# Kernel tuning notes

Hardware: AMD Instinct MI355X
Metric: run time of the kernel (lower is better)

The kernel has to match this reference:

```python
import jax, jax.numpy as jnp
import numpy as np

B = 16384
D = 64            # bottom_mlp_layers[-1] = embedding_dim
DENSE = 512
HIST = 50         # history length per row
C_CAMP = 1000     # num_collisions for campaign table (sqrt(1e6))
C_FEAT = 316      # num_collisions for 1e5-vocab tables
NQ_CAMP = 1000    # ceil(1e6/1000)
NQ_FEAT = 317     # ceil(1e5/316)
NFEAT = 7
N = NFEAT + 1 + 1 # sparse features + dense row
PROJ = 128


def setup_inputs() -> dict:
    key = jax.random.key(0)
    ks = jax.random.split(key, 20)
    inp = {
        'x': jax.random.normal(ks[0], (B, DENSE), jnp.float32),
        'hist_idx': jax.random.randint(ks[1], (B * HIST,), 0, 1000000),
        'hist_offsets': jnp.arange(B, dtype=jnp.int64) * HIST,
        'feat_idx': jax.random.randint(ks[2], (B, NFEAT), 0, 100000),
        # QR embedding tables (quotient, remainder)
        'Wq_c': jax.random.normal(ks[3], (NQ_CAMP, D), jnp.float32) * 0.05,
        'Wr_c': jax.random.normal(ks[4], (C_CAMP, D), jnp.float32) * 0.05,
        'Wq_f': jax.random.normal(ks[5], (NFEAT, NQ_FEAT, D), jnp.float32) * 0.05,
        'Wr_f': jax.random.normal(ks[6], (NFEAT, C_FEAT, D), jnp.float32) * 0.05,
        # bottom MLP: 512->512 relu 512->256 relu 256->64
        'W0': jax.random.normal(ks[7], (512, DENSE), jnp.float32) * 0.03,
        'b0': jnp.zeros((512,), jnp.float32),
        'W1': jax.random.normal(ks[8], (256, 512), jnp.float32) * 0.04,
        'b1': jnp.zeros((256,), jnp.float32),
        'W2': jax.random.normal(ks[9], (64, 256), jnp.float32) * 0.06,
        'b2': jnp.zeros((64,), jnp.float32),
        # projection: (D + (N^2-N)/2) -> PROJ ; 64 + 36 = 100
        'Wp': jax.random.normal(ks[10], (PROJ, D + (N * N - N) // 2), jnp.float32) * 0.1,
        'bp': jnp.zeros((PROJ,), jnp.float32),
    }
    return inp


def _forward(x, hist_idx, hist_offsets, feat_idx, Wq_c, Wr_c, Wq_f, Wr_f,
             W0, b0, W1, b1, W2, b2, Wp, bp):
    # bottom MLP
    h = jax.nn.relu(x @ W0.T + b0)
    h = jax.nn.relu(h @ W1.T + b1)
    dense = h @ W2.T + b2                                   # [B, D]

    # QR embedding bag (mode='mean', operation='mult') for history feature
    e = Wq_c[hist_idx // C_CAMP] * Wr_c[hist_idx % C_CAMP]  # [M, D]
    M = hist_idx.shape[0]
    seg = jnp.cumsum(jnp.zeros((M,), jnp.int32).at[hist_offsets].add(1)) - 1
    sums = jax.ops.segment_sum(e, seg, num_segments=B)      # [B, D]
    counts = jnp.diff(jnp.concatenate([hist_offsets, jnp.array([M], hist_offsets.dtype)]))
    hist_emb = sums / counts[:, None].astype(sums.dtype)

    # single-valued QR lookups (bag size 1 -> mean == lookup)
    t = jnp.arange(NFEAT)[None, :]
    fe = Wq_f[t, feat_idx // C_FEAT] * Wr_f[t, feat_idx % C_FEAT]  # [B, NFEAT, D]

    # pairwise dot interaction: upper triangle (offset=1) of T @ T^T
    T = jnp.concatenate([dense[:, None, :], hist_emb[:, None, :], fe], axis=1)  # [B, N, D]
    Z = jnp.einsum('bnd,bmd->bnm', T, T)
    row, col = np.triu_indices(N, k=1)
    Z_flat = Z[:, row, col]                                  # [B, (N^2-N)/2]

    combined = jnp.concatenate([dense, Z_flat], axis=1)
    return combined @ Wp.T + bp                              # [B, PROJ]


def reference(x, hist_idx, hist_offsets, feat_idx, Wq_c, Wr_c, Wq_f, Wr_f,
              W0, b0, W1, b1, W2, b2, Wp, bp):
    return _forward(x, hist_idx, hist_offsets, feat_idx, Wq_c, Wr_c, Wq_f, Wr_f,
                    W0, b0, W1, b1, W2, b2, Wp, bp)
```

## Files before the change

kernel.cpp:

```cpp
#include <hip/hip_runtime.h>
#include <hip/hip_bf16.h>
#include <stdint.h>

#define DENSE_D 512
#define HIDDEN1 512
#define HIDDEN2 256
#define EMB_D   64
#define NFEAT   7
#define NROWS   9
#define NPAIRS  36
#define COMB    100
#define KPROJ   128
#define PROJ    128
#define C_CAMP  1000
#define C_FEAT  316
#define NQ_FEAT 317

typedef __attribute__((ext_vector_type(8))) __bf16 bf16x8;
typedef __attribute__((ext_vector_type(8))) unsigned short ushort8;
typedef __attribute__((ext_vector_type(4))) float  facc4;

#define GLD_LDS16(gp, lp) __builtin_amdgcn_global_load_lds( \
    (__attribute__((address_space(1))) void*)(gp), \
    (__attribute__((address_space(3))) void*)(lp), 16, 0, 0)

__device__ inline unsigned short f2bf(float f) {
    __hip_bfloat16 h = __float2bfloat16(f);
    return *reinterpret_cast<unsigned short*>(&h);
}
__device__ inline float blo(unsigned int u) { return __uint_as_float(u << 16); }
__device__ inline float bhi(unsigned int u) { return __uint_as_float(u & 0xffff0000u); }

template<int BM, int BN, int WM, int WN, bool RELU, bool OUT_BF16, bool A_F32>
__global__ __launch_bounds__(WM * WN * 64)
void gemm_bf16(const void* __restrict__ Avoid,
               const __hip_bfloat16* __restrict__ W,
               const float* __restrict__ bias,
               void* __restrict__ Cout,
               int M, int N, int K)
{
    constexpr int BK      = 32;
    constexpr int THREADS = WM * WN * 64;
    constexpr int MREP    = BM / (WM * 16);
    constexpr int NREP    = BN / (WN * 16);
    constexpr int ACH     = BM * BK / 8;
    constexpr int BCH     = BN * BK / 8;

    __shared__ __align__(16) __hip_bfloat16 Asm[BK / 8][BM][8];
    __shared__ __align__(16) __hip_bfloat16 Bsm[BK / 8][BN][8];

    const int tid  = threadIdx.x;
    const int lane = tid & 63;
    const int wave = tid >> 6;
    const int wm   = wave / WN;
    const int wn   = wave % WN;
    const int row0 = blockIdx.x * BM;
    const int col0 = blockIdx.y * BN;
    const int fr   = lane & 15;
    const int fk   = lane >> 4;

    facc4 acc[MREP][NREP] = {};

    for (int k0 = 0; k0 < K; k0 += BK) {
        if (A_F32) {
            const float* Af = (const float*)Avoid;
            for (int p = tid; p < ACH; p += THREADS) {
                const int r  = p & (BM - 1);
                const int kc = p / BM;
                const float* src = Af + (size_t)(row0 + r) * K + k0 + kc * 8;
                const float4 v0 = *reinterpret_cast<const float4*>(src);
                const float4 v1 = *reinterpret_cast<const float4*>(src + 4);
                ushort8 cv;
                cv[0] = f2bf(v0.x); cv[1] = f2bf(v0.y);
                cv[2] = f2bf(v0.z); cv[3] = f2bf(v0.w);
                cv[4] = f2bf(v1.x); cv[5] = f2bf(v1.y);
                cv[6] = f2bf(v1.z); cv[7] = f2bf(v1.w);
                *reinterpret_cast<ushort8*>(
                    (unsigned short*)(&Asm[0][0][0]) + (size_t)p * 8) = cv;
            }
        } else {
            const __hip_bfloat16* Ab = (const __hip_bfloat16*)Avoid;
            for (int p = tid; p < ACH; p += THREADS) {
                const int r  = p & (BM - 1);
                const int kc = p / BM;
                GLD_LDS16(Ab + (size_t)(row0 + r) * K + k0 + kc * 8,
                          (&Asm[0][0][0]) + (size_t)p * 8);
            }
        }
        for (int p = tid; p < BCH; p += THREADS) {
            const int r  = p & (BN - 1);
            const int kc = p / BN;
            GLD_LDS16(W + (size_t)(col0 + r) * K + k0 + kc * 8,
                      (&Bsm[0][0][0]) + (size_t)p * 8);
        }
        __syncthreads();

        bf16x8 af[MREP], bw[NREP];
        #pragma unroll
        for (int m = 0; m < MREP; ++m)
            af[m] = *reinterpret_cast<const bf16x8*>(
                &Asm[fk][wm * (MREP * 16) + m * 16 + fr][0]);
        #pragma unroll
        for (int n = 0; n < NREP; ++n)
            bw[n] = *reinterpret_cast<const bf16x8*>(
                &Bsm[fk][wn * (NREP * 16) + n * 16 + fr][0]);
        #pragma unroll
        for (int m = 0; m < MREP; ++m)
            #pragma unroll
            for (int n = 0; n < NREP; ++n)
                acc[m][n] = __builtin_amdgcn_mfma_f32_16x16x32_bf16(
                    af[m], bw[n], acc[m][n], 0, 0, 0);
        __syncthreads();
    }

    #pragma unroll
    for (int n = 0; n < NREP; ++n) {
        const int col = col0 + wn * (NREP * 16) + n * 16 + fr;
        const float bv = bias[col];
        #pragma unroll
        for (int m = 0; m < MREP; ++m) {
            #pragma unroll
            for (int j = 0; j < 4; ++j) {
                const int row = row0 + wm * (MREP * 16) + m * 16 + fk * 4 + j;
                float v = acc[m][n][j] + bv;
                if (RELU) v = fmaxf(v, 0.f);
                if (OUT_BF16)
                    ((__hip_bfloat16*)Cout)[(size_t)row * N + col] = __float2bfloat16(v);
                else
                    ((float*)Cout)[(size_t)row * N + col] = v;
            }
        }
    }
}

__device__ inline void cast_seg(const float* __restrict__ src,
                                unsigned short* __restrict__ dst,
                                int n4, int id, int stride)
{
    for (int i = id; i < n4; i += stride) {
        const float4 v = reinterpret_cast<const float4*>(src)[i];
        ushort4 o;
        o.x = f2bf(v.x); o.y = f2bf(v.y); o.z = f2bf(v.z); o.w = f2bf(v.w);
        reinterpret_cast<ushort4*>(dst)[i] = o;
    }
}

__global__ __launch_bounds__(256)
void prep_all(const float* __restrict__ W0, const float* __restrict__ W1,
              const float* __restrict__ W2, const float* __restrict__ Wp,
              const float* __restrict__ Wq_c, const float* __restrict__ Wr_c,
              const float* __restrict__ Wq_f, const float* __restrict__ Wr_f,
              unsigned short* w0b, unsigned short* w1b, unsigned short* w2b,
              unsigned short* wpb, unsigned short* qcb, unsigned short* rcb,
              unsigned short* qfb, unsigned short* rfb)
{
    const int id = blockIdx.x * blockDim.x + threadIdx.x;
    const int stride = gridDim.x * blockDim.x;
    cast_seg(W0,   w0b, HIDDEN1 * DENSE_D / 4, id, stride);
    cast_seg(W1,   w1b, HIDDEN2 * HIDDEN1 / 4, id, stride);
    cast_seg(W2,   w2b, EMB_D * HIDDEN2 / 4,   id, stride);
    cast_seg(Wq_c, qcb, C_CAMP * EMB_D / 4,    id, stride);
    cast_seg(Wr_c, rcb, C_CAMP * EMB_D / 4,    id, stride);
    cast_seg(Wq_f, qfb, NFEAT * NQ_FEAT * EMB_D / 4, id, stride);
    cast_seg(Wr_f, rfb, NFEAT * C_FEAT * EMB_D / 4,  id, stride);
    for (int i = id; i < PROJ * KPROJ; i += stride) {
        const int r = i >> 7, c = i & 127;
        wpb[i] = (c < COMB) ? f2bf(Wp[r * COMB + c]) : (unsigned short)0;
    }
}

__global__ __launch_bounds__(256)
void tail_fused(const unsigned short* __restrict__ h1b,
                const unsigned short* __restrict__ w2b,
                const float* __restrict__ b2,
                const int* __restrict__ hist_idx,
                const int* __restrict__ hist_off,
                const int* __restrict__ feat_idx,
                const unsigned short* __restrict__ qcb,
                const unsigned short* __restrict__ rcb,
                const unsigned short* __restrict__ qfb,
                const unsigned short* __restrict__ rfb,
                const unsigned short* __restrict__ wpb,
                const float* __restrict__ bp,
                float* __restrict__ out,
                int B, int Mtot)
{
    const int r0   = blockIdx.x * 32;
    const int t    = threadIdx.x;
    const int lane = t & 63;
    const int wave = t >> 6;
    const int wm   = wave >> 1;
    const int wn   = wave & 1;
    const int fr   = lane & 15;
    const int fk   = lane >> 4;

    __shared__ unsigned short T[32][NROWS][68];
    __shared__ unsigned short combs[32][136];

    {
        facc4 acc[2] = {};
        const unsigned short* arow = h1b + (size_t)(r0 + wm * 16 + fr) * HIDDEN2;
        #pragma unroll
        for (int kw = 0; kw < 8; ++kw) {
            const bf16x8 af = *reinterpret_cast<const bf16x8*>(arow + kw * 32 + fk * 8);
            #pragma unroll
            for (int n = 0; n < 2; ++n) {
                const bf16x8 bw = *reinterpret_cast<const bf16x8*>(
                    w2b + (size_t)(wn * 32 + n * 16 + fr) * HIDDEN2 + kw * 32 + fk * 8);
                acc[n] = __builtin_amdgcn_mfma_f32_16x16x32_bf16(af, bw, acc[n], 0, 0, 0);
            }
        }
        #pragma unroll
        for (int n = 0; n < 2; ++n) {
            const int col = wn * 32 + n * 16 + fr;
            const float bv = b2[col];
            #pragma unroll
            for (int j = 0; j < 4; ++j) {
                const int row = wm * 16 + fk * 4 + j;
                const unsigned short hv = f2bf(acc[n][j] + bv);
                T[row][0][col]  = hv;
                combs[row][col] = hv;
            }
        }
    }

    for (int p = t; p < 32 * 18; p += 256) {
        const int row = p / 18, c = p % 18;
        *reinterpret_cast<unsigned int*>(&combs[row][100 + c * 2]) = 0u;
    }

    {
        const int row = t >> 3;
        const int oc  = t & 7;
        const int br  = r0 + row;

        const int fbase = br * NFEAT;
        #pragma unroll
        for (int f = 0; f < NFEAT; ++f) {
            const int fi = feat_idx[fbase + f];
            const int q = fi / C_FEAT, r = fi - q * C_FEAT;
            const unsigned short* qp = qfb + ((size_t)f * NQ_FEAT + q) * EMB_D + oc * 8;
            const unsigned short* rp = rfb + ((size_t)f * C_FEAT  + r) * EMB_D + oc * 8;
            const uint2 qa = *reinterpret_cast<const uint2*>(qp);
            const uint2 qb = *reinterpret_cast<const uint2*>(qp + 4);
            const uint2 ra = *reinterpret_cast<const uint2*>(rp);
            const uint2 rb = *reinterpret_cast<const uint2*>(rp + 4);
            union { ushort8 v; uint2 u[2]; } pk;
            pk.v[0] = f2bf(blo(qa.x) * blo(ra.x));
            pk.v[1] = f2bf(bhi(qa.x) * bhi(ra.x));
            pk.v[2] = f2bf(blo(qa.y) * blo(ra.y));
            pk.v[3] = f2bf(bhi(qa.y) * bhi(ra.y));
            pk.v[4] = f2bf(blo(qb.x) * blo(rb.x));
            pk.v[5] = f2bf(bhi(qb.x) * bhi(rb.x));
            pk.v[6] = f2bf(blo(qb.y) * blo(rb.y));
            pk.v[7] = f2bf(bhi(qb.y) * bhi(rb.y));
            *reinterpret_cast<uint2*>(&T[row][2 + f][oc * 8])     = pk.u[0];
            *reinterpret_cast<uint2*>(&T[row][2 + f][oc * 8 + 4]) = pk.u[1];
        }

        const int start = hist_off[br];
        const int end   = (br + 1 < B) ? hist_off[br + 1] : Mtot;
        const int cnt   = end - start;
        const int* hp = hist_idx + start;
        float a[8] = {};
        #pragma unroll 2
        for (int i = 0; i < cnt; ++i) {
            const int hi = hp[i];
            const int q = hi / C_CAMP, r = hi - q * C_CAMP;
            const unsigned short* qp = qcb + (size_t)q * EMB_D + oc * 8;
            const unsigned short* rp = rcb + (size_t)r * EMB_D + oc * 8;
            const uint2 qa = *reinterpret_cast<const uint2*>(qp);
            const uint2 qb = *reinterpret_cast<const uint2*>(qp + 4);
            const uint2 ra = *reinterpret_cast<const uint2*>(rp);
            const uint2 rb = *reinterpret_cast<const uint2*>(rp + 4);
            a[0] += blo(qa.x) * blo(ra.x); a[1] += bhi(qa.x) * bhi(ra.x);
            a[2] += blo(qa.y) * blo(ra.y); a[3] += bhi(qa.y) * bhi(ra.y);
            a[4] += blo(qb.x) * blo(rb.x); a[5] += bhi(qb.x) * bhi(rb.x);
            a[6] += blo(qb.y) * blo(rb.y); a[7] += bhi(qb.y) * bhi(rb.y);
        }
        const float inv = 1.f / (float)max(cnt, 1);
        union { ushort8 v; uint2 u[2]; } pk;
        #pragma unroll
        for (int k = 0; k < 8; ++k) pk.v[k] = f2bf(a[k] * inv);
        *reinterpret_cast<uint2*>(&T[row][1][oc * 8])     = pk.u[0];
        *reinterpret_cast<uint2*>(&T[row][1][oc * 8 + 4]) = pk.u[1];
    }
    __syncthreads();

    for (int p = t; p < NPAIRS * 32; p += 256) {
        const int row = p & 31;
        const int pr  = p >> 5;
        int i = 0, rem = pr;
        while (rem >= (NROWS - 1) - i) { rem -= (NROWS - 1) - i; ++i; }
        const int j = i + 1 + rem;
        const unsigned short* ti = &T[row][i][0];
        const unsigned short* tj = &T[row][j][0];
        float s = 0.f;
        #pragma unroll
        for (int d = 0; d < EMB_D; d += 4) {
            const uint2 u = *reinterpret_cast<const uint2*>(ti + d);
            const uint2 v = *reinterpret_cast<const uint2*>(tj + d);
            s += blo(u.x) * blo(v.x) + bhi(u.x) * bhi(v.x)
               + blo(u.y) * blo(v.y) + bhi(u.y) * bhi(v.y);
        }
        combs[row][EMB_D + pr] = f2bf(s);
    }
    __syncthreads();

    {
        facc4 acc[4] = {};
        #pragma unroll
        for (int kw = 0; kw < 4; ++kw) {
            const bf16x8 af = *reinterpret_cast<const bf16x8*>(
                &combs[wm * 16 + fr][kw * 32 + fk * 8]);
            #pragma unroll
            for (int n = 0; n < 4; ++n) {
                const bf16x8 bw = *reinterpret_cast<const bf16x8*>(
                    wpb + (size_t)(wn * 64 + n * 16 + fr) * KPROJ + kw * 32 + fk * 8);
                acc[n] = __builtin_amdgcn_mfma_f32_16x16x32_bf16(af, bw, acc[n], 0, 0, 0);
            }
        }
        #pragma unroll
        for (int n = 0; n < 4; ++n) {
            const int col = wn * 64 + n * 16 + fr;
            const float bv = bp[col];
            #pragma unroll
            for (int j = 0; j < 4; ++j) {
                const int row = wm * 16 + fk * 4 + j;
                out[(size_t)(r0 + row) * PROJ + col] = acc[n][j] + bv;
            }
        }
    }
}

extern "C" void kernel_launch(void* const* d_in, const int* in_sizes, int n_in,
                              void* d_out, int out_size, void* d_ws, size_t ws_size,
                              hipStream_t stream)
{
    const float* x        = (const float*)d_in[0];
    const int*   hist_idx = (const int*)  d_in[1];
    const int*   hist_off = (const int*)  d_in[2];
    const int*   feat_idx = (const int*)  d_in[3];
    const float* Wq_c     = (const float*)d_in[4];
    const float* Wr_c     = (const float*)d_in[5];
    const float* Wq_f     = (const float*)d_in[6];
    const float* Wr_f     = (const float*)d_in[7];
    const float* W0       = (const float*)d_in[8];
    const float* b0       = (const float*)d_in[9];
    const float* W1       = (const float*)d_in[10];
    const float* b1       = (const float*)d_in[11];
    const float* W2       = (const float*)d_in[12];
    const float* b2       = (const float*)d_in[13];
    const float* Wp       = (const float*)d_in[14];
    const float* bp       = (const float*)d_in[15];

    const int M    = in_sizes[0] / DENSE_D;
    const int Mtot = in_sizes[1];

    char* w = (char*)d_ws;
    auto take = [&](size_t bytes) { char* p = w; w += (bytes + 255) & ~(size_t)255; return p; };
    unsigned short* w0b = (unsigned short*)take(HIDDEN1 * DENSE_D * 2);
    unsigned short* w1b = (unsigned short*)take(HIDDEN2 * HIDDEN1 * 2);
    unsigned short* w2b = (unsigned short*)take(EMB_D * HIDDEN2 * 2);
    unsigned short* wpb = (unsigned short*)take(PROJ * KPROJ * 2);
    unsigned short* qcb = (unsigned short*)take(C_CAMP * EMB_D * 2);
    unsigned short* rcb = (unsigned short*)take(C_CAMP * EMB_D * 2);
    unsigned short* qfb = (unsigned short*)take(NFEAT * NQ_FEAT * EMB_D * 2);
    unsigned short* rfb = (unsigned short*)take(NFEAT * C_FEAT * EMB_D * 2);
    unsigned short* h0b = (unsigned short*)take((size_t)M * HIDDEN1 * 2);
    unsigned short* h1b = (unsigned short*)take((size_t)M * HIDDEN2 * 2);

    prep_all<<<512, 256, 0, stream>>>(W0, W1, W2, Wp, Wq_c, Wr_c, Wq_f, Wr_f,
                                      w0b, w1b, w2b, wpb, qcb, rcb, qfb, rfb);

    gemm_bf16<128, 256, 2, 4, true, true, true>
        <<<dim3(M / 128, HIDDEN1 / 256), 512, 0, stream>>>(
        x, (const __hip_bfloat16*)w0b, b0, h0b, M, HIDDEN1, DENSE_D);

    gemm_bf16<64, 256, 2, 4, true, true, false>
        <<<dim3(M / 64, HIDDEN2 / 256), 512, 0, stream>>>(
        h0b, (const __hip_bfloat16*)w1b, b1, h1b, M, HIDDEN2, HIDDEN1);

    tail_fused<<<M / 32, 256, 0, stream>>>(
        h1b, w2b, b2, hist_idx, hist_off, feat_idx,
        qcb, rcb, qfb, rfb, wpb, bp, (float*)d_out, M, Mtot);
}
```

Before: 87.67 us.

## Switch MLP GEMMs to 32x32 MFMA full-width tiles and halve tail block rows

The bottom-MLP GEMMs now use 32x32x16 bf16 MFMA. Each block covers the full output width (64 rows by 512 or 256 columns), with the 8 waves split only along N, so the fp32 x tile is loaded and converted once instead of once per column tile. The fused tail kernel now handles 16 rows per block instead of 32, with 16 threads per row for the gathers. This doubles the block count for latency hiding, but each wave does fewer MFMAs per gather. The risk is that larger accumulators (16 floats per fragment, MREP=2 by NREP=2) raise register pressure and may lower occupancy.

```diff
diff --git a/kernel.cpp b/kernel.cpp
--- a/kernel.cpp
+++ b/kernel.cpp
@@ -15,10 +15,12 @@
 #define C_CAMP  1000
 #define C_FEAT  316
 #define NQ_FEAT 317
-
-typedef __attribute__((ext_vector_type(8))) __bf16 bf16x8;
-typedef __attribute__((ext_vector_type(8))) unsigned short ushort8;
-typedef __attribute__((ext_vector_type(4))) float  facc4;
+#define TROWS   16
+
+typedef __attribute__((ext_vector_type(8)))  __bf16 bf16x8;
+typedef __attribute__((ext_vector_type(8)))  unsigned short ushort8;
+typedef __attribute__((ext_vector_type(4)))  float  facc4;
+typedef __attribute__((ext_vector_type(16))) float  facc16;
 
 #define GLD_LDS16(gp, lp) __builtin_amdgcn_global_load_lds( \
     (__attribute__((address_space(1))) void*)(gp), \
@@ -31,18 +33,18 @@
 __device__ inline float blo(unsigned int u) { return __uint_as_float(u << 16); }
 __device__ inline float bhi(unsigned int u) { return __uint_as_float(u & 0xffff0000u); }
 
-template<int BM, int BN, int WM, int WN, bool RELU, bool OUT_BF16, bool A_F32>
-__global__ __launch_bounds__(WM * WN * 64)
-void gemm_bf16(const void* __restrict__ Avoid,
-               const __hip_bfloat16* __restrict__ W,
-               const float* __restrict__ bias,
-               void* __restrict__ Cout,
-               int M, int N, int K)
+template<int BM, int BN, int WN, bool RELU, bool OUT_BF16, bool A_F32>
+__global__ __launch_bounds__(WN * 64)
+void gemm32(const void* __restrict__ Avoid,
+            const __hip_bfloat16* __restrict__ W,
+            const float* __restrict__ bias,
+            void* __restrict__ Cout,
+            int M, int N, int K)
 {
     constexpr int BK      = 32;
-    constexpr int THREADS = WM * WN * 64;
-    constexpr int MREP    = BM / (WM * 16);
-    constexpr int NREP    = BN / (WN * 16);
+    constexpr int THREADS = WN * 64;
+    constexpr int MREP    = BM / 32;
+    constexpr int NREP    = BN / (WN * 32);
     constexpr int ACH     = BM * BK / 8;
     constexpr int BCH     = BN * BK / 8;
 
@@ -52,14 +54,12 @@
     const int tid  = threadIdx.x;
     const int lane = tid & 63;
     const int wave = tid >> 6;
-    const int wm   = wave / WN;
-    const int wn   = wave % WN;
     const int row0 = blockIdx.x * BM;
     const int col0 = blockIdx.y * BN;
-    const int fr   = lane & 15;
-    const int fk   = lane >> 4;
-
-    facc4 acc[MREP][NREP] = {};
+    const int fr   = lane & 31;
+    const int fh   = lane >> 5;
+
+    facc16 acc[MREP][NREP] = {};
 
     for (int k0 = 0; k0 < K; k0 += BK) {
         if (A_F32) {
@@ -95,34 +95,39 @@
         }
         __syncthreads();
 
-        bf16x8 af[MREP], bw[NREP];
-        #pragma unroll
-        for (int m = 0; m < MREP; ++m)
-            af[m] = *reinterpret_cast<const bf16x8*>(
-                &Asm[fk][wm * (MREP * 16) + m * 16 + fr][0]);
-        #pragma unroll
-        for (int n = 0; n < NREP; ++n)
-            bw[n] = *reinterpret_cast<const bf16x8*>(
-                &Bsm[fk][wn * (NREP * 16) + n * 16 + fr][0]);
-        #pragma unroll
-        for (int m = 0; m < MREP; ++m)
+        bf16x8 af[2][MREP], bw[2][NREP];
+        #pragma unroll
+        for (int s = 0; s < 2; ++s) {
+            #pragma unroll
+            for (int m = 0; m < MREP; ++m)
+                af[s][m] = *reinterpret_cast<const bf16x8*>(
+                    &Asm[s * 2 + fh][m * 32 + fr][0]);
             #pragma unroll
             for (int n = 0; n < NREP; ++n)
-                acc[m][n] = __builtin_amdgcn_mfma_f32_16x16x32_bf16(
-                    af[m], bw[n], acc[m][n], 0, 0, 0);
+                bw[s][n] = *reinterpret_cast<const bf16x8*>(
+                    &Bsm[s * 2 + fh][wave * (NREP * 32) + n * 32 + fr][0]);
+        }
+        #pragma unroll
+        for (int s = 0; s < 2; ++s)
+            #pragma unroll
+            for (int m = 0; m < MREP; ++m)
+                #pragma unroll
+                for (int n = 0; n < NREP; ++n)
+                    acc[m][n] = __builtin_amdgcn_mfma_f32_32x32x16_bf16(
+                        af[s][m], bw[s][n], acc[m][n], 0, 0, 0);
         __syncthreads();
     }
 
     #pragma unroll
     for (int n = 0; n < NREP; ++n) {
-        const int col = col0 + wn * (NREP * 16) + n * 16 + fr;
+        const int col = col0 + wave * (NREP * 32) + n * 32 + fr;
         const float bv = bias[col];
         #pragma unroll
         for (int m = 0; m < MREP; ++m) {
             #pragma unroll
-            for (int j = 0; j < 4; ++j) {
-                const int row = row0 + wm * (MREP * 16) + m * 16 + fk * 4 + j;
-                float v = acc[m][n][j] + bv;
+            for (int r = 0; r < 16; ++r) {
+                const int row = row0 + m * 32 + (r & 3) + 8 * (r >> 2) + 4 * fh;
+                float v = acc[m][n][r] + bv;
                 if (RELU) v = fmaxf(v, 0.f);
                 if (OUT_BF16)
                     ((__hip_bfloat16*)Cout)[(size_t)row * N + col] = __float2bfloat16(v);
@@ -185,53 +190,45 @@
                 float* __restrict__ out,
                 int B, int Mtot)
 {
-    const int r0   = blockIdx.x * 32;
+    const int r0   = blockIdx.x * TROWS;
     const int t    = threadIdx.x;
     const int lane = t & 63;
     const int wave = t >> 6;
-    const int wm   = wave >> 1;
-    const int wn   = wave & 1;
     const int fr   = lane & 15;
     const int fk   = lane >> 4;
 
-    __shared__ unsigned short T[32][NROWS][68];
-    __shared__ unsigned short combs[32][136];
+    __shared__ __align__(16) unsigned short T[TROWS][NROWS][68];
+    __shared__ __align__(16) unsigned short combs[TROWS][136];
 
     {
-        facc4 acc[2] = {};
-        const unsigned short* arow = h1b + (size_t)(r0 + wm * 16 + fr) * HIDDEN2;
+        facc4 acc = {};
+        const unsigned short* arow = h1b + (size_t)(r0 + fr) * HIDDEN2;
+        const unsigned short* brow = w2b + (size_t)(wave * 16 + fr) * HIDDEN2;
         #pragma unroll
         for (int kw = 0; kw < 8; ++kw) {
             const bf16x8 af = *reinterpret_cast<const bf16x8*>(arow + kw * 32 + fk * 8);
-            #pragma unroll
-            for (int n = 0; n < 2; ++n) {
-                const bf16x8 bw = *reinterpret_cast<const bf16x8*>(
-                    w2b + (size_t)(wn * 32 + n * 16 + fr) * HIDDEN2 + kw * 32 + fk * 8);
-                acc[n] = __builtin_amdgcn_mfma_f32_16x16x32_bf16(af, bw, acc[n], 0, 0, 0);
-            }
-        }
-        #pragma unroll
-        for (int n = 0; n < 2; ++n) {
-            const int col = wn * 32 + n * 16 + fr;
-            const float bv = b2[col];
-            #pragma unroll
-            for (int j = 0; j < 4; ++j) {
-                const int row = wm * 16 + fk * 4 + j;
-                const unsigned short hv = f2bf(acc[n][j] + bv);
-                T[row][0][col]  = hv;
-                combs[row][col] = hv;
-            }
-        }
-    }
-
-    for (int p = t; p < 32 * 18; p += 256) {
+            const bf16x8 bw = *reinterpret_cast<const bf16x8*>(brow + kw * 32 + fk * 8);
+            acc = __builtin_amdgcn_mfma_f32_16x16x32_bf16(af, bw, acc, 0, 0, 0);
+        }
+        const int col = wave * 16 + fr;
+        const float bv = b2[col];
+        #pragma unroll
+        for (int j = 0; j < 4; ++j) {
+            const int row = fk * 4 + j;
+            const unsigned short hv = f2bf(acc[j] + bv);
+            T[row][0][col]  = hv;
+            combs[row][col] = hv;
+        }
+    }
+
+    for (int p = t; p < TROWS * 18; p += 256) {
         const int row = p / 18, c = p % 18;
         *reinterpret_cast<unsigned int*>(&combs[row][100 + c * 2]) = 0u;
     }
 
     {
-        const int row = t >> 3;
-        const int oc  = t & 7;
+        const int row = t >> 4;
+        const int oc  = t & 15;
         const int br  = r0 + row;
 
         const int fbase = br * NFEAT;
@@ -239,57 +236,45 @@
         for (int f = 0; f < NFEAT; ++f) {
             const int fi = feat_idx[fbase + f];
             const int q = fi / C_FEAT, r = fi - q * C_FEAT;
-            const unsigned short* qp = qfb + ((size_t)f * NQ_FEAT + q) * EMB_D + oc * 8;
-            const unsigned short* rp = rfb + ((size_t)f * C_FEAT  + r) * EMB_D + oc * 8;
-            const uint2 qa = *reinterpret_cast<const uint2*>(qp);
-            const uint2 qb = *reinterpret_cast<const uint2*>(qp + 4);
-            const uint2 ra = *reinterpret_cast<const uint2*>(rp);
-            const uint2 rb = *reinterpret_cast<const uint2*>(rp + 4);
-            union { ushort8 v; uint2 u[2]; } pk;
-            pk.v[0] = f2bf(blo(qa.x) * blo(ra.x));
-            pk.v[1] = f2bf(bhi(qa.x) * bhi(ra.x));
-            pk.v[2] = f2bf(blo(qa.y) * blo(ra.y));
-            pk.v[3] = f2bf(bhi(qa.y) * bhi(ra.y));
-            pk.v[4] = f2bf(blo(qb.x) * blo(rb.x));
-            pk.v[5] = f2bf(bhi(qb.x) * bhi(rb.x));
-            pk.v[6] = f2bf(blo(qb.y) * blo(rb.y));
-            pk.v[7] = f2bf(bhi(qb.y) * bhi(rb.y));
-            *reinterpret_cast<uint2*>(&T[row][2 + f][oc * 8])     = pk.u[0];
-            *reinterpret_cast<uint2*>(&T[row][2 + f][oc * 8 + 4]) = pk.u[1];
+            const uint2 qv = *reinterpret_cast<const uint2*>(
+                qfb + ((size_t)f * NQ_FEAT + q) * EMB_D + oc * 4);
+            const uint2 rv = *reinterpret_cast<const uint2*>(
+                rfb + ((size_t)f * C_FEAT + r) * EMB_D + oc * 4);
+            union { ushort4 v; uint2 u; } pk;
+            pk.v.x = f2bf(blo(qv.x) * blo(rv.x));
+            pk.v.y = f2bf(bhi(qv.x) * bhi(rv.x));
+            pk.v.z = f2bf(blo(qv.y) * blo(rv.y));
+            pk.v.w = f2bf(bhi(qv.y) * bhi(rv.y));
+            *reinterpret_cast<uint2*>(&T[row][2 + f][oc * 4]) = pk.u;
         }
 
         const int start = hist_off[br];
         const int end   = (br + 1 < B) ? hist_off[br + 1] : Mtot;
         const int cnt   = end - start;
         const int* hp = hist_idx + start;
-        float a[8] = {};
+        float a0 = 0.f, a1 = 0.f, a2 = 0.f, a3 = 0.f;
         #pragma unroll 2
         for (int i = 0; i < cnt; ++i) {
             const int hi = hp[i];
             const int q = hi / C_CAMP, r = hi - q * C_CAMP;
-            const unsigned short* qp = qcb + (size_t)q * EMB_D + oc * 8;
-            const unsigned short* rp = rcb + (size_t)r * EMB_D + oc * 8;
-            const uint2 qa = *reinterpret_cast<const uint2*>(qp);
-            const uint2 qb = *reinterpret_cast<const uint2*>(qp + 4);
-            const uint2 ra = *reinterpret_cast<const uint2*>(rp);
-            const uint2 rb = *reinterpret_cast<const uint2*>(rp + 4);
-            a[0] += blo(qa.x) * blo(ra.x); a[1] += bhi(qa.x) * bhi(ra.x);
-            a[2] += blo(qa.y) * blo(ra.y); a[3] += bhi(qa.y) * bhi(ra.y);
-            a[4] += blo(qb.x) * blo(rb.x); a[5] += bhi(qb.x) * bhi(rb.x);
-            a[6] += blo(qb.y) * blo(rb.y); a[7] += bhi(qb.y) * bhi(rb.y);
+            const uint2 qv = *reinterpret_cast<const uint2*>(qcb + (size_t)q * EMB_D + oc * 4);
+            const uint2 rv = *reinterpret_cast<const uint2*>(rcb + (size_t)r * EMB_D + oc * 4);
+            a0 += blo(qv.x) * blo(rv.x);
+            a1 += bhi(qv.x) * bhi(rv.x);
+            a2 += blo(qv.y) * blo(rv.y);
+            a3 += bhi(qv.y) * bhi(rv.y);
         }
         const float inv = 1.f / (float)max(cnt, 1);
-        union { ushort8 v; uint2 u[2]; } pk;
-        #pragma unroll
-        for (int k = 0; k < 8; ++k) pk.v[k] = f2bf(a[k] * inv);
-        *reinterpret_cast<uint2*>(&T[row][1][oc * 8])     = pk.u[0];
-        *reinterpret_cast<uint2*>(&T[row][1][oc * 8 + 4]) = pk.u[1];
+        union { ushort4 v; uint2 u; } pk;
+        pk.v.x = f2bf(a0 * inv); pk.v.y = f2bf(a1 * inv);
+        pk.v.z = f2bf(a2 * inv); pk.v.w = f2bf(a3 * inv);
+        *reinterpret_cast<uint2*>(&T[row][1][oc * 4]) = pk.u;
     }
     __syncthreads();
 
-    for (int p = t; p < NPAIRS * 32; p += 256) {
-        const int row = p & 31;
-        const int pr  = p >> 5;
+    for (int p = t; p < NPAIRS * TROWS; p += 256) {
+        const int row = p & (TROWS - 1);
+        const int pr  = p / TROWS;
         int i = 0, rem = pr;
         while (rem >= (NROWS - 1) - i) { rem -= (NROWS - 1) - i; ++i; }
         const int j = i + 1 + rem;
@@ -308,25 +293,25 @@
     __syncthreads();
 
     {
-        facc4 acc[4] = {};
+        facc4 acc[2] = {};
         #pragma unroll
         for (int kw = 0; kw < 4; ++kw) {
             const bf16x8 af = *reinterpret_cast<const bf16x8*>(
-                &combs[wm * 16 + fr][kw * 32 + fk * 8]);
-            #pragma unroll
-            for (int n = 0; n < 4; ++n) {
+                &combs[fr][kw * 32 + fk * 8]);
+            #pragma unroll
+            for (int n = 0; n < 2; ++n) {
                 const bf16x8 bw = *reinterpret_cast<const bf16x8*>(
-                    wpb + (size_t)(wn * 64 + n * 16 + fr) * KPROJ + kw * 32 + fk * 8);
+                    wpb + (size_t)(wave * 32 + n * 16 + fr) * KPROJ + kw * 32 + fk * 8);
                 acc[n] = __builtin_amdgcn_mfma_f32_16x16x32_bf16(af, bw, acc[n], 0, 0, 0);
             }
         }
         #pragma unroll
-        for (int n = 0; n < 4; ++n) {
-            const int col = wn * 64 + n * 16 + fr;
+        for (int n = 0; n < 2; ++n) {
+            const int col = wave * 32 + n * 16 + fr;
             const float bv = bp[col];
             #pragma unroll
             for (int j = 0; j < 4; ++j) {
-                const int row = wm * 16 + fk * 4 + j;
+                const int row = fk * 4 + j;
                 out[(size_t)(r0 + row) * PROJ + col] = acc[n][j] + bv;
             }
         }
@@ -373,15 +358,15 @@
     prep_all<<<512, 256, 0, stream>>>(W0, W1, W2, Wp, Wq_c, Wr_c, Wq_f, Wr_f,
                                       w0b, w1b, w2b, wpb, qcb, rcb, qfb, rfb);
 
-    gemm_bf16<128, 256, 2, 4, true, true, true>
-        <<<dim3(M / 128, HIDDEN1 / 256), 512, 0, stream>>>(
+    gemm32<64, 512, 8, true, true, true>
+        <<<dim3(M / 64, 1), 512, 0, stream>>>(
         x, (const __hip_bfloat16*)w0b, b0, h0b, M, HIDDEN1, DENSE_D);
 
-    gemm_bf16<64, 256, 2, 4, true, true, false>
-        <<<dim3(M / 64, HIDDEN2 / 256), 512, 0, stream>>>(
+    gemm32<64, 256, 8, true, true, false>
+        <<<dim3(M / 64, 1), 512, 0, stream>>>(
         h0b, (const __hip_bfloat16*)w1b, b1, h1b, M, HIDDEN2, HIDDEN1);
 
-    tail_fused<<<M / 32, 256, 0, stream>>>(
+    tail_fused<<<M / TROWS, 256, 0, stream>>>(
         h1b, w2b, b2, hist_idx, hist_off, feat_idx,
         qcb, rcb, qfb, rfb, wpb, bp, (float*)d_out, M, Mtot);
 }
```

New measurement: 98.58 us. 1.12x slower.
